# Optimization experiments

Measured on AMD Instinct MI355X. Metric: run time of the kernel, lower is better.

The kernel has to match this reference:

```python
import jax, jax.numpy as jnp
import numpy as np

WINDOW = 7
PAD = WINDOW // 2
EPS = 1e-8  # torch F.cosine_similarity default eps


def setup_inputs() -> dict:
    key = jax.random.key(0)
    k1, k2, k3 = jax.random.split(key, 3)
    b, c, h, w = 4, 128, 96, 96
    reduced = max(c // 4, 16)  # 32
    x = jax.random.normal(k1, (b, c, h, w), dtype=jnp.float32)
    # 1x1 conv weights (kaiming-uniform-ish scale)
    W_reduce = jax.random.uniform(k2, (reduced, c), dtype=jnp.float32, minval=-1.0, maxval=1.0) * (1.0 / np.sqrt(c))
    W_proj = jax.random.uniform(k3, (c, reduced), dtype=jnp.float32, minval=-1.0, maxval=1.0) * (1.0 / np.sqrt(reduced))
    return {"x": x, "W_reduce": W_reduce, "W_proj": W_proj}


def _local_patches(feat, h, w):
    # feat: (b, r, h, w) -> (b, r, window^2, h, w), unfold ordering (row-major kernel)
    padded = jnp.pad(feat, ((0, 0), (0, 0), (PAD, PAD), (PAD, PAD)))
    return jnp.stack(
        [padded[:, :, i:i + h, j:j + w] for i in range(WINDOW) for j in range(WINDOW)],
        axis=2,
    )


def reference(x, W_reduce, W_proj):
    b, c, h, w = x.shape
    # 1x1 conv reduce
    feat = jnp.einsum('rc,bchw->brhw', W_reduce, x)  # (b, r, h, w)
    patches = _local_patches(feat, h, w)             # (b, r, k2, h, w)
    # cosine similarity along channel dim between center and each patch
    dot = jnp.einsum('brhw,brkhw->bkhw', feat, patches)
    n_center = jnp.sqrt(jnp.sum(feat * feat, axis=1))[:, None]        # (b,1,h,w)
    n_patch = jnp.sqrt(jnp.sum(patches * patches, axis=1))            # (b,k2,h,w)
    sim = dot / jnp.maximum(n_center * n_patch, EPS)                  # (b,k2,h,w)
    att = jax.nn.softmax(sim, axis=1)                                 # over window dim
    corr = jnp.einsum('bkhw,brkhw->brhw', att, patches)               # (b,r,h,w)
    enhanced = jnp.einsum('cr,brhw->bchw', W_proj, corr)              # 1x1 conv proj
    return x + enhanced
```

## Files before the change

### kernel.cpp

```cpp
#include <hip/hip_runtime.h>

#define BB 4
#define CC 128
#define HH 96
#define WWX 96
#define RED 32
#define HW (HH * WWX)
#define NPIX (BB * HW)
#define PADW 3
#define EPSC 1e-8f

__global__ __launch_bounds__(256) void reduce_kern(
    const float* __restrict__ x, const float* __restrict__ Wr,
    float* __restrict__ feat, float* __restrict__ norms) {
  __shared__ float part[3][64][33];
  int lane = threadIdx.x & 63;
  int cg = __builtin_amdgcn_readfirstlane(threadIdx.x >> 6);
  int pix = blockIdx.x * 64 + lane;
  int b = pix / HW;
  int p = pix - b * HW;
  const float* xp = x + (size_t)b * CC * HW + p;

  float acc[RED];
#pragma unroll
  for (int r = 0; r < RED; ++r) acc[r] = 0.f;

#pragma unroll 4
  for (int i = 0; i < CC / 4; ++i) {
    int c = cg * (CC / 4) + i;
    float xv = xp[(size_t)c * HW];
#pragma unroll
    for (int r = 0; r < RED; ++r) acc[r] = fmaf(Wr[r * CC + c], xv, acc[r]);
  }

  if (cg != 0) {
#pragma unroll
    for (int r = 0; r < RED; ++r) part[cg - 1][lane][r] = acc[r];
  }
  __syncthreads();
  if (cg == 0) {
#pragma unroll
    for (int g = 0; g < 3; ++g)
#pragma unroll
      for (int r = 0; r < RED; ++r) acc[r] += part[g][lane][r];

    float ss = 0.f;
#pragma unroll
    for (int r = 0; r < RED; ++r) ss = fmaf(acc[r], acc[r], ss);
    norms[pix] = sqrtf(ss);

    float4* fo = (float4*)(feat + (size_t)pix * RED);
#pragma unroll
    for (int r4 = 0; r4 < RED / 4; ++r4)
      fo[r4] = make_float4(acc[4 * r4], acc[4 * r4 + 1], acc[4 * r4 + 2], acc[4 * r4 + 3]);
  }
}

__global__ __launch_bounds__(256) void corr_kern(
    const float* __restrict__ x, const float* __restrict__ Wp,
    const float* __restrict__ feat, const float* __restrict__ norms,
    float* __restrict__ out) {
  __shared__ float cbuf[64][33];
  int tid = threadIdx.x;
  int rg = tid & 3;
  int q = tid >> 2;
  int px = q & 31, py = q >> 5;
  int gx = blockIdx.x * 32 + px;
  int gy = blockIdx.y * 2 + py;
  int b = blockIdx.z;
  int pix = b * HW + gy * WWX + gx;

  float f[8];
  {
    const float4* fc = (const float4*)(feat + (size_t)pix * RED + rg * 8);
    float4 t0 = fc[0], t1 = fc[1];
    f[0] = t0.x; f[1] = t0.y; f[2] = t0.z; f[3] = t0.w;
    f[4] = t1.x; f[5] = t1.y; f[6] = t1.z; f[7] = t1.w;
  }
  float nc = norms[pix];

  float corr[8];
#pragma unroll
  for (int r = 0; r < 8; ++r) corr[r] = 0.f;
  float l = 0.f;

#pragma unroll
  for (int dy = -PADW; dy <= PADW; ++dy) {
    int yy = gy + dy;
    bool rowok = ((unsigned)yy < HH);
#pragma unroll
    for (int dx = -PADW; dx <= PADW; ++dx) {
      int xx = gx + dx;
      if (rowok && ((unsigned)xx < WWX)) {
        int npx = b * HW + yy * WWX + xx;
        const float4* fn = (const float4*)(feat + (size_t)npx * RED + rg * 8);
        float4 v0 = fn[0], v1 = fn[1];
        float v[8];
        v[0] = v0.x; v[1] = v0.y; v[2] = v0.z; v[3] = v0.w;
        v[4] = v1.x; v[5] = v1.y; v[6] = v1.z; v[7] = v1.w;
        float dot = 0.f;
#pragma unroll
        for (int r = 0; r < 8; ++r) dot = fmaf(f[r], v[r], dot);
        dot += __shfl_xor(dot, 1);
        dot += __shfl_xor(dot, 2);
        float np = norms[npx];
        float sim = dot * __builtin_amdgcn_rcpf(fmaxf(nc * np, EPSC));
        float wgt = __expf(sim);
        l += wgt;
#pragma unroll
        for (int r = 0; r < 8; ++r) corr[r] = fmaf(wgt, v[r], corr[r]);
      } else {
        l += 1.f;
      }
    }
  }

  float invl = __builtin_amdgcn_rcpf(l);
#pragma unroll
  for (int r = 0; r < 8; ++r) cbuf[q][rg * 8 + r] = corr[r] * invl;
  __syncthreads();

  int p2 = tid & 63;
  int cg = __builtin_amdgcn_readfirstlane(tid >> 6);
  int px2 = p2 & 31, py2 = p2 >> 5;
  int pp = (blockIdx.y * 2 + py2) * WWX + blockIdx.x * 32 + px2;

  float cr[RED];
#pragma unroll
  for (int r = 0; r < RED; ++r) cr[r] = cbuf[p2][r];

  const float* xc = x + (size_t)b * CC * HW + pp;
  float* oc = out + (size_t)b * CC * HW + pp;
#pragma unroll 4
  for (int i = 0; i < CC / 4; ++i) {
    int c = cg * (CC / 4) + i;
    float a = xc[(size_t)c * HW];
#pragma unroll
    for (int r = 0; r < RED; ++r) a = fmaf(Wp[c * RED + r], cr[r], a);
    oc[(size_t)c * HW] = a;
  }
}

extern "C" void kernel_launch(void* const* d_in, const int* in_sizes, int n_in,
                              void* d_out, int out_size, void* d_ws, size_t ws_size,
                              hipStream_t stream) {
  const float* x  = (const float*)d_in[0];
  const float* Wr = (const float*)d_in[1];
  const float* Wp = (const float*)d_in[2];
  float* out = (float*)d_out;

  float* feat  = (float*)d_ws;
  float* norms = feat + (size_t)NPIX * RED;

  reduce_kern<<<NPIX / 64, 256, 0, stream>>>(x, Wr, feat, norms);

  dim3 g(WWX / 32, HH / 2, BB);
  corr_kern<<<g, 256, 0, stream>>>(x, Wp, feat, norms, out);
}
```

Before: 123.6 us.

## Stage neighborhood features and norms in shared memory for correlation kernel

The correlation kernel now cooperatively loads a 38x8 halo tile of reduced features and norms into LDS, then reads all 49 neighbours from shared memory instead of global/L2. Out-of-bounds halo entries are zero-filled, so zero vectors give sim=0 and weight 1, matching the old padding path without branches. It adds about 45KB of LDS per block, which may limit occupancy, and the halo is redundantly loaded (2-row tile with 6 rows of halo). It also raises the unroll factor in the reduce kernel.

```diff
diff --git a/kernel.cpp b/kernel.cpp
--- a/kernel.cpp
+++ b/kernel.cpp
@@ -7,8 +7,14 @@
 #define RED 32
 #define HW (HH * WWX)
 #define NPIX (BB * HW)
-#define PADW 3
 #define EPSC 1e-8f
+
+#define TX 32
+#define TY 2
+#define HX 38
+#define HY 8
+#define NHALO (HX * HY)
+#define PSTRIDE 36
 
 __global__ __launch_bounds__(256) void reduce_kern(
     const float* __restrict__ x, const float* __restrict__ Wr,
@@ -25,7 +31,7 @@
 #pragma unroll
   for (int r = 0; r < RED; ++r) acc[r] = 0.f;
 
-#pragma unroll 4
+#pragma unroll 8
   for (int i = 0; i < CC / 4; ++i) {
     int c = cg * (CC / 4) + i;
     float xv = xp[(size_t)c * HW];
@@ -60,24 +66,43 @@
     const float* __restrict__ x, const float* __restrict__ Wp,
     const float* __restrict__ feat, const float* __restrict__ norms,
     float* __restrict__ out) {
+  __shared__ float fbuf[NHALO * PSTRIDE];
+  __shared__ float nbuf[NHALO];
   __shared__ float cbuf[64][33];
   int tid = threadIdx.x;
+  int b = blockIdx.z;
+  int bx = blockIdx.x * TX, by = blockIdx.y * TY;
+
+  for (int s = tid; s < NHALO * 8; s += 256) {
+    int px = s >> 3, part = s & 7;
+    int hy = px / HX, hx = px - hy * HX;
+    int gy = by - 3 + hy, gx = bx - 3 + hx;
+    float4 v = make_float4(0.f, 0.f, 0.f, 0.f);
+    if ((unsigned)gy < HH && (unsigned)gx < WWX)
+      v = *(const float4*)(feat + (size_t)(b * HW + gy * WWX + gx) * RED + part * 4);
+    *(float4*)(fbuf + px * PSTRIDE + part * 4) = v;
+  }
+  for (int n = tid; n < NHALO; n += 256) {
+    int hy = n / HX, hx = n - hy * HX;
+    int gy = by - 3 + hy, gx = bx - 3 + hx;
+    nbuf[n] = ((unsigned)gy < HH && (unsigned)gx < WWX)
+                  ? norms[b * HW + gy * WWX + gx] : 0.f;
+  }
+  __syncthreads();
+
   int rg = tid & 3;
   int q = tid >> 2;
-  int px = q & 31, py = q >> 5;
-  int gx = blockIdx.x * 32 + px;
-  int gy = blockIdx.y * 2 + py;
-  int b = blockIdx.z;
-  int pix = b * HW + gy * WWX + gx;
+  int px1 = q & 31, py1 = q >> 5;
+  int hidx = (py1 + 3) * HX + (px1 + 3);
 
   float f[8];
   {
-    const float4* fc = (const float4*)(feat + (size_t)pix * RED + rg * 8);
+    const float4* fc = (const float4*)(fbuf + hidx * PSTRIDE + rg * 8);
     float4 t0 = fc[0], t1 = fc[1];
     f[0] = t0.x; f[1] = t0.y; f[2] = t0.z; f[3] = t0.w;
     f[4] = t1.x; f[5] = t1.y; f[6] = t1.z; f[7] = t1.w;
   }
-  float nc = norms[pix];
+  float nc = nbuf[hidx];
 
   float corr[8];
 #pragma unroll
@@ -85,33 +110,26 @@
   float l = 0.f;
 
 #pragma unroll
-  for (int dy = -PADW; dy <= PADW; ++dy) {
-    int yy = gy + dy;
-    bool rowok = ((unsigned)yy < HH);
+  for (int dy = -3; dy <= 3; ++dy) {
 #pragma unroll
-    for (int dx = -PADW; dx <= PADW; ++dx) {
-      int xx = gx + dx;
-      if (rowok && ((unsigned)xx < WWX)) {
-        int npx = b * HW + yy * WWX + xx;
-        const float4* fn = (const float4*)(feat + (size_t)npx * RED + rg * 8);
-        float4 v0 = fn[0], v1 = fn[1];
-        float v[8];
-        v[0] = v0.x; v[1] = v0.y; v[2] = v0.z; v[3] = v0.w;
-        v[4] = v1.x; v[5] = v1.y; v[6] = v1.z; v[7] = v1.w;
-        float dot = 0.f;
+    for (int dx = -3; dx <= 3; ++dx) {
+      int ho = hidx + dy * HX + dx;
+      const float4* fn = (const float4*)(fbuf + ho * PSTRIDE + rg * 8);
+      float4 v0 = fn[0], v1 = fn[1];
+      float v[8];
+      v[0] = v0.x; v[1] = v0.y; v[2] = v0.z; v[3] = v0.w;
+      v[4] = v1.x; v[5] = v1.y; v[6] = v1.z; v[7] = v1.w;
+      float dot = 0.f;
 #pragma unroll
-        for (int r = 0; r < 8; ++r) dot = fmaf(f[r], v[r], dot);
-        dot += __shfl_xor(dot, 1);
-        dot += __shfl_xor(dot, 2);
-        float np = norms[npx];
-        float sim = dot * __builtin_amdgcn_rcpf(fmaxf(nc * np, EPSC));
-        float wgt = __expf(sim);
-        l += wgt;
+      for (int r = 0; r < 8; ++r) dot = fmaf(f[r], v[r], dot);
+      dot += __shfl_xor(dot, 1);
+      dot += __shfl_xor(dot, 2);
+      float np = nbuf[ho];
+      float sim = dot * __builtin_amdgcn_rcpf(fmaxf(nc * np, EPSC));
+      float wgt = __expf(sim);
+      l += wgt;
 #pragma unroll
-        for (int r = 0; r < 8; ++r) corr[r] = fmaf(wgt, v[r], corr[r]);
-      } else {
-        l += 1.f;
-      }
+      for (int r = 0; r < 8; ++r) corr[r] = fmaf(wgt, v[r], corr[r]);
     }
   }
 
@@ -123,7 +141,7 @@
   int p2 = tid & 63;
   int cg = __builtin_amdgcn_readfirstlane(tid >> 6);
   int px2 = p2 & 31, py2 = p2 >> 5;
-  int pp = (blockIdx.y * 2 + py2) * WWX + blockIdx.x * 32 + px2;
+  int pp = (by + py2) * WWX + bx + px2;
 
   float cr[RED];
 #pragma unroll
@@ -154,6 +172,6 @@
 
   reduce_kern<<<NPIX / 64, 256, 0, stream>>>(x, Wr, feat, norms);
 
-  dim3 g(WWX / 32, HH / 2, BB);
+  dim3 g(WWX / TX, HH / TY, BB);
   corr_kern<<<g, 256, 0, stream>>>(x, Wp, feat, norms, out);
 }
```

Result: no change. 122.3 us (-1.1%).
